# Optimization experiments

Hardware: AMD Instinct MI355X
Metric: run time of the kernel (lower is better)

Reference implementation:

```python
import jax, jax.numpy as jnp
import numpy as np


def setup_inputs() -> dict:
    key = jax.random.key(0)
    ks = jax.random.split(key, 5)
    B, E, P, K, F = 4096, 8, 256, 16, 64  # batch, experts, num_patches, patch_dim, filter_size
    x = jax.random.normal(ks[0], (B, 1, P * K), dtype=jnp.float32)
    noise = jax.random.uniform(ks[1], (B, 1), dtype=jnp.float32)  # torch.rand(B, 1)
    gw = jnp.zeros((E, K), dtype=jnp.float32)  # gating weight zeroed in __init__
    gb = (jax.random.uniform(ks[2], (E,), dtype=jnp.float32) * 2.0 - 1.0) / np.float32(np.sqrt(K))
    ew = jax.random.normal(ks[3], (E, 2 * F, K), dtype=jnp.float32) * 1e-4  # small_init
    eb = jax.random.normal(ks[4], (E, 2 * F), dtype=jnp.float32) * 1e-4
    return {"x": x, "noise": noise, "gw": gw, "gb": gb, "ew": ew, "eb": eb}


def reference(x, noise, gw, gb, ew, eb):
    # Conv1d with kernel==stride==K and in_channels=1 is patch-extract + matmul.
    B = x.shape[0]
    E, K = gw.shape
    L = x.shape[2]
    P = L // K
    F2 = ew.shape[1]
    F = F2 // 2
    xp = x.reshape(B, P, K)  # [B, P, K] patches
    # gating: conv then sum over patch positions (bias contributes P times)
    h = jnp.einsum('bpk,ek->be', xp, gw) + P * gb + noise  # [B, E]
    # top-1 routing
    pi_val = jnp.max(h, axis=-1, keepdims=True)  # [B, 1]
    pi_idx = jnp.argmax(h, axis=-1)  # [B]
    mask = jax.nn.one_hot(pi_idx, E, dtype=x.dtype)  # [B, E]
    loss = (h.mean(axis=0) * mask.mean(axis=0)).mean() * float(E * E)
    # dense one-hot dispatch (faithful to 'bnd,ben->ebd' with n==1)
    expert_in = jnp.einsum('bpk,be->ebpk', xp, mask)  # [E, B, P, K]
    # per-expert conv (linear=True, no cubic act) + sum over patches; bias sums P times
    y = jnp.einsum('ebpk,efk->ebf', expert_in, ew) + P * eb[:, None, :]  # [E, B, 2F]
    out_e = jnp.stack([y[..., :F].sum(-1), y[..., F:].sum(-1)], axis=-1)  # [E, B, 2]
    combine = pi_val * mask  # [B, E]
    output = jnp.einsum('be,ebj->bj', combine, out_e)  # [B, 2]
    return (output, mask, loss)
```

## Files before the change

kernel.cpp:

```cpp
#include <hip/hip_runtime.h>
#include <math.h>

#define BB 4096
#define NE 8
#define NP 256
#define NK 16
#define NF 64
#define ROW 4096

#define WS_W 0
#define WS_B 256
#define WS_H 272
#define WS_M 8464
#define NBLK 1024

__global__ __launch_bounds__(256) void prep_kernel(const float* __restrict__ ew,
                                                   const float* __restrict__ eb,
                                                   float* __restrict__ ws) {
    int t = threadIdx.x;
    int e = t >> 5, j = (t >> 4) & 1, k = t & 15;
    const float* base = ew + e * (128 * 16) + j * (64 * 16) + k;
    float s = 0.f;
#pragma unroll
    for (int f = 0; f < 64; ++f) s += base[f * 16];
    ws[WS_W + t] = s;
    if (t < 16) {
        int e2 = t >> 1, j2 = t & 1;
        const float* bb = eb + e2 * 128 + j2 * 64;
        float sb = 0.f;
#pragma unroll
        for (int f = 0; f < 64; ++f) sb += bb[f];
        ws[WS_B + t] = sb;
    }
}

__global__ __launch_bounds__(256) void main_kernel(const float* __restrict__ x,
                                                   const float* __restrict__ noise,
                                                   const float* __restrict__ gw,
                                                   const float* __restrict__ gb,
                                                   const float* __restrict__ ws,
                                                   float* __restrict__ out,
                                                   float* __restrict__ hpart,
                                                   float* __restrict__ mpart) {
    __shared__ float s_sh[4][16];
    __shared__ float hacc[8];
    __shared__ float macc[8];
    int tid = threadIdx.x;
    if (tid < 8) { hacc[tid] = 0.f; macc[tid] = 0.f; }
    __syncthreads();

    int wave = tid >> 6;
    int lane = tid & 63;
    int b = blockIdx.x * 4 + wave;

    const float4* xb = (const float4*)(x + (size_t)b * ROW);
    float4 acc = make_float4(0.f, 0.f, 0.f, 0.f);
#pragma unroll
    for (int t = 0; t < 16; ++t) {
        float4 v = xb[lane + 64 * t];
        acc.x += v.x; acc.y += v.y; acc.z += v.z; acc.w += v.w;
    }
#pragma unroll
    for (int m = 4; m <= 32; m <<= 1) {
        acc.x += __shfl_xor(acc.x, m);
        acc.y += __shfl_xor(acc.y, m);
        acc.z += __shfl_xor(acc.z, m);
        acc.w += __shfl_xor(acc.w, m);
    }
    if (lane < 4) {
        s_sh[wave][4 * lane + 0] = acc.x;
        s_sh[wave][4 * lane + 1] = acc.y;
        s_sh[wave][4 * lane + 2] = acc.z;
        s_sh[wave][4 * lane + 3] = acc.w;
    }
    __builtin_amdgcn_wave_barrier();

    float hv = -3.0e38f;
    if (lane < 8) {
        const float* gwr = gw + lane * NK;
        float d = 0.f;
#pragma unroll
        for (int k = 0; k < NK; ++k) d += s_sh[wave][k] * gwr[k];
        hv = d + 256.f * gb[lane] + noise[b];
    }
    float mv = hv;
    int mi = lane & 7;
#pragma unroll
    for (int m = 1; m <= 4; m <<= 1) {
        float ov = __shfl_xor(mv, m);
        int oi = __shfl_xor(mi, m);
        if (ov > mv || (ov == mv && oi < mi)) { mv = ov; mi = oi; }
    }

    if (lane == 0) {
        const float* Wr = ws + WS_W + mi * 32;
        const float* Bs = ws + WS_B + mi * 2;
        float o0 = 0.f, o1 = 0.f;
#pragma unroll
        for (int k = 0; k < NK; ++k) {
            float sv = s_sh[wave][k];
            o0 += sv * Wr[k];
            o1 += sv * Wr[16 + k];
        }
        o0 = mv * (o0 + 256.f * Bs[0]);
        o1 = mv * (o1 + 256.f * Bs[1]);
        out[b * 2 + 0] = o0;
        out[b * 2 + 1] = o1;
    }
    if (lane < 8) {
        float mk = (lane == mi) ? 1.f : 0.f;
        out[2 * BB + b * 8 + lane] = mk;
        atomicAdd(&hacc[lane], hv);
        atomicAdd(&macc[lane], mk);
    }
    __syncthreads();
    if (tid < 8) {
        hpart[blockIdx.x * 8 + tid] = hacc[tid];
        mpart[blockIdx.x * 8 + tid] = macc[tid];
    }
}

__global__ __launch_bounds__(256) void loss_kernel(const float* __restrict__ hpart,
                                                   const float* __restrict__ mpart,
                                                   float* __restrict__ out) {
    __shared__ float hs[256], ms[256];
    int t = threadIdx.x;
    int e = t & 7, c = t >> 3;
    float hsum = 0.f, msum = 0.f;
    for (int i = c; i < NBLK; i += 32) {
        hsum += hpart[i * 8 + e];
        msum += mpart[i * 8 + e];
    }
    hs[t] = hsum;
    ms[t] = msum;
    __syncthreads();
    if (t < 8) {
        float hh = 0.f, mm = 0.f;
        for (int c2 = 0; c2 < 32; ++c2) { hh += hs[c2 * 8 + t]; mm += ms[c2 * 8 + t]; }
        hs[t] = hh;
        ms[t] = mm;
    }
    __syncthreads();
    if (t == 0) {
        float loss = 0.f;
        for (int e2 = 0; e2 < 8; ++e2)
            loss += (hs[e2] / 4096.f) * (ms[e2] / 4096.f);
        out[2 * BB + 8 * BB] = loss * 8.f;
    }
}

extern "C" void kernel_launch(void* const* d_in, const int* in_sizes, int n_in,
                              void* d_out, int out_size, void* d_ws, size_t ws_size,
                              hipStream_t stream) {
    const float* x     = (const float*)d_in[0];
    const float* noise = (const float*)d_in[1];
    const float* gw    = (const float*)d_in[2];
    const float* gb    = (const float*)d_in[3];
    const float* ew    = (const float*)d_in[4];
    const float* eb    = (const float*)d_in[5];
    float* out = (float*)d_out;
    float* ws  = (float*)d_ws;

    prep_kernel<<<1, 256, 0, stream>>>(ew, eb, ws);
    main_kernel<<<NBLK, 256, 0, stream>>>(x, noise, gw, gb, ws, out,
                                          ws + WS_H, ws + WS_M);
    loss_kernel<<<1, 256, 0, stream>>>(ws + WS_H, ws + WS_M, out);
}
```

Before: 122.0 us.

## Fuse loss reduction into main kernel via last-block atomic counter

Removes the separate loss kernel launch. Each block stores its per-expert partial sums with release semantics and increments a global counter, and the last block to arrive reduces all partials and writes the loss. Patch sums are now broadcast through register shuffles instead of shared memory. This saves one kernel launch and its gap, but adds an atomic counter and a serial final reduction done by a single block.

```diff
diff --git a/kernel.cpp b/kernel.cpp
--- a/kernel.cpp
+++ b/kernel.cpp
@@ -7,12 +7,12 @@
 #define NK 16
 #define NF 64
 #define ROW 4096
+#define NBLK 1024
 
-#define WS_W 0
-#define WS_B 256
-#define WS_H 272
-#define WS_M 8464
-#define NBLK 1024
+#define WS_W   0
+#define WS_B   256
+#define WS_CNT 272
+#define WS_P   288
 
 __global__ __launch_bounds__(256) void prep_kernel(const float* __restrict__ ew,
                                                    const float* __restrict__ eb,
@@ -32,21 +32,21 @@
         for (int f = 0; f < 64; ++f) sb += bb[f];
         ws[WS_B + t] = sb;
     }
+    if (t == 0) *(int*)(ws + WS_CNT) = 0;
 }
 
-__global__ __launch_bounds__(256) void main_kernel(const float* __restrict__ x,
-                                                   const float* __restrict__ noise,
-                                                   const float* __restrict__ gw,
-                                                   const float* __restrict__ gb,
-                                                   const float* __restrict__ ws,
-                                                   float* __restrict__ out,
-                                                   float* __restrict__ hpart,
-                                                   float* __restrict__ mpart) {
-    __shared__ float s_sh[4][16];
+__global__ __launch_bounds__(256) void fused_kernel(const float* __restrict__ x,
+                                                    const float* __restrict__ noise,
+                                                    const float* __restrict__ gw,
+                                                    const float* __restrict__ gb,
+                                                    float* __restrict__ ws,
+                                                    float* __restrict__ out) {
     __shared__ float hacc[8];
     __shared__ float macc[8];
+    __shared__ int lastflag;
     int tid = threadIdx.x;
     if (tid < 8) { hacc[tid] = 0.f; macc[tid] = 0.f; }
+    if (tid == 0) lastflag = 0;
     __syncthreads();
 
     int wave = tid >> 6;
@@ -67,20 +67,21 @@
         acc.z += __shfl_xor(acc.z, m);
         acc.w += __shfl_xor(acc.w, m);
     }
-    if (lane < 4) {
-        s_sh[wave][4 * lane + 0] = acc.x;
-        s_sh[wave][4 * lane + 1] = acc.y;
-        s_sh[wave][4 * lane + 2] = acc.z;
-        s_sh[wave][4 * lane + 3] = acc.w;
+    float s[16];
+#pragma unroll
+    for (int q = 0; q < 4; ++q) {
+        s[4 * q + 0] = __shfl(acc.x, q);
+        s[4 * q + 1] = __shfl(acc.y, q);
+        s[4 * q + 2] = __shfl(acc.z, q);
+        s[4 * q + 3] = __shfl(acc.w, q);
     }
-    __builtin_amdgcn_wave_barrier();
 
     float hv = -3.0e38f;
     if (lane < 8) {
         const float* gwr = gw + lane * NK;
         float d = 0.f;
 #pragma unroll
-        for (int k = 0; k < NK; ++k) d += s_sh[wave][k] * gwr[k];
+        for (int k = 0; k < NK; ++k) d += s[k] * gwr[k];
         hv = d + 256.f * gb[lane] + noise[b];
     }
     float mv = hv;
@@ -98,14 +99,12 @@
         float o0 = 0.f, o1 = 0.f;
 #pragma unroll
         for (int k = 0; k < NK; ++k) {
-            float sv = s_sh[wave][k];
+            float sv = s[k];
             o0 += sv * Wr[k];
             o1 += sv * Wr[16 + k];
         }
-        o0 = mv * (o0 + 256.f * Bs[0]);
-        o1 = mv * (o1 + 256.f * Bs[1]);
-        out[b * 2 + 0] = o0;
-        out[b * 2 + 1] = o1;
+        out[b * 2 + 0] = mv * (o0 + 256.f * Bs[0]);
+        out[b * 2 + 1] = mv * (o1 + 256.f * Bs[1]);
     }
     if (lane < 8) {
         float mk = (lane == mi) ? 1.f : 0.f;
@@ -114,38 +113,49 @@
         atomicAdd(&macc[lane], mk);
     }
     __syncthreads();
+
+    float* part = ws + WS_P;
     if (tid < 8) {
-        hpart[blockIdx.x * 8 + tid] = hacc[tid];
-        mpart[blockIdx.x * 8 + tid] = macc[tid];
-    }
-}
-
-__global__ __launch_bounds__(256) void loss_kernel(const float* __restrict__ hpart,
-                                                   const float* __restrict__ mpart,
-                                                   float* __restrict__ out) {
-    __shared__ float hs[256], ms[256];
-    int t = threadIdx.x;
-    int e = t & 7, c = t >> 3;
-    float hsum = 0.f, msum = 0.f;
-    for (int i = c; i < NBLK; i += 32) {
-        hsum += hpart[i * 8 + e];
-        msum += mpart[i * 8 + e];
-    }
-    hs[t] = hsum;
-    ms[t] = msum;
-    __syncthreads();
-    if (t < 8) {
-        float hh = 0.f, mm = 0.f;
-        for (int c2 = 0; c2 < 32; ++c2) { hh += hs[c2 * 8 + t]; mm += ms[c2 * 8 + t]; }
-        hs[t] = hh;
-        ms[t] = mm;
+        __hip_atomic_store(&part[blockIdx.x * 16 + tid], hacc[tid],
+                           __ATOMIC_RELEASE, __HIP_MEMORY_SCOPE_AGENT);
+    } else if (tid < 16) {
+        __hip_atomic_store(&part[blockIdx.x * 16 + tid], macc[tid - 8],
+                           __ATOMIC_RELEASE, __HIP_MEMORY_SCOPE_AGENT);
     }
     __syncthreads();
-    if (t == 0) {
-        float loss = 0.f;
-        for (int e2 = 0; e2 < 8; ++e2)
-            loss += (hs[e2] / 4096.f) * (ms[e2] / 4096.f);
-        out[2 * BB + 8 * BB] = loss * 8.f;
+    if (tid == 0) {
+        __threadfence();
+        int old = atomicAdd((int*)(ws + WS_CNT), 1);
+        if (old == NBLK - 1) lastflag = 1;
+    }
+    __syncthreads();
+
+    if (lastflag) {
+        __shared__ float red[16][17];
+        int e = tid & 15, c = tid >> 4;
+        float sum = 0.f;
+        for (int blk = c; blk < NBLK; blk += 16)
+            sum += __hip_atomic_load(&part[blk * 16 + e],
+                                     __ATOMIC_ACQUIRE, __HIP_MEMORY_SCOPE_AGENT);
+        red[c][e] = sum;
+        __syncthreads();
+        if (tid == 0) {
+            float hs[8], ms[8];
+#pragma unroll
+            for (int e2 = 0; e2 < 8; ++e2) { hs[e2] = 0.f; ms[e2] = 0.f; }
+            for (int c2 = 0; c2 < 16; ++c2) {
+#pragma unroll
+                for (int e2 = 0; e2 < 8; ++e2) {
+                    hs[e2] += red[c2][e2];
+                    ms[e2] += red[c2][8 + e2];
+                }
+            }
+            float loss = 0.f;
+#pragma unroll
+            for (int e2 = 0; e2 < 8; ++e2)
+                loss += (hs[e2] / 4096.f) * (ms[e2] / 4096.f);
+            out[2 * BB + 8 * BB] = loss * 8.f;
+        }
     }
 }
 
@@ -162,7 +172,5 @@
     float* ws  = (float*)d_ws;
 
     prep_kernel<<<1, 256, 0, stream>>>(ew, eb, ws);
-    main_kernel<<<NBLK, 256, 0, stream>>>(x, noise, gw, gb, ws, out,
-                                          ws + WS_H, ws + WS_M);
-    loss_kernel<<<1, 256, 0, stream>>>(ws + WS_H, ws + WS_M, out);
+    fused_kernel<<<NBLK, 256, 0, stream>>>(x, noise, gw, gb, ws, out);
 }
```

After: 195.3 us. +60.1%, slower.
